# Performance work log

Measured on AMD Instinct MI355X. Metric: run time of the kernel, lower is better.

The kernel has to match this reference:

```python
import jax, jax.numpy as jnp
import numpy as np

H = 8
LN_EPS = 1e-5


def _layer_norm(t):
    # LayerNorm over last dim, no affine (elementwise_affine=False, bias=False)
    mu = jnp.mean(t, axis=-1, keepdims=True)
    var = jnp.var(t, axis=-1, keepdims=True)
    return (t - mu) / jnp.sqrt(var + LN_EPS)


def setup_inputs() -> dict:
    key = jax.random.key(0)
    ks = jax.random.split(key, 7)
    B, N, D, K = 2, 8192, 512, 32
    x = jax.random.normal(ks[0], (B, N, D), dtype=jnp.float32)
    idx = jax.random.randint(ks[1], (N, K), 0, N)
    s = 1.0 / np.sqrt(D)  # kaiming-ish init scale for stability
    Wq = jax.random.normal(ks[2], (D, D), dtype=jnp.float32) * s
    Wk = jax.random.normal(ks[3], (D, D), dtype=jnp.float32) * s
    Wv = jax.random.normal(ks[4], (D, D), dtype=jnp.float32) * s
    Wout = jax.random.normal(ks[5], (D, D), dtype=jnp.float32) * s
    bout = jnp.zeros((D,), dtype=jnp.float32)
    return {"x": x, "idx": idx, "Wq": Wq, "Wk": Wk, "Wv": Wv, "Wout": Wout, "bout": bout}


def reference(x, idx, Wq, Wk, Wv, Wout, bout):
    B, N, D = x.shape
    d_k = D // H

    def proj(W):
        # torch Linear: x @ W.T ; reshape to (B, H, N, d_k)
        return (x @ W.T).reshape(B, N, H, d_k).transpose(0, 2, 1, 3)

    Q, K, V = proj(Wq), proj(Wk), proj(Wv)
    # per-head LayerNorm on d_k (all heads identical since no affine params)
    Q = _layer_norm(Q)
    K = _layer_norm(K)

    # grouped (neighborhood) attention: gather K,V at neighbor indices
    Kg = K[:, :, idx]  # (B, H, N, k, d_k)
    Vg = V[:, :, idx]  # (B, H, N, k, d_k)
    scores = jnp.einsum('bhnd,bhnkd->bhnk', Q, Kg) / jnp.sqrt(jnp.asarray(d_k, x.dtype))
    attn = jax.nn.softmax(scores, axis=-1)
    out = jnp.einsum('bhnk,bhnkd->bhnd', attn, Vg)  # (B, H, N, d_k)

    out = out.transpose(0, 2, 1, 3).reshape(B, N, D)
    return out @ Wout.T + bout
```

## Files before the change

kernel.cpp:

```cpp
#include <hip/hip_runtime.h>
#include <hip/hip_bf16.h>
#include <math.h>

#define BB 2
#define NN 8192
#define DD 512
#define HH 8
#define DK 64
#define KNB 32
#define BN (BB*NN)
#define BHN (BB*HH*NN)

typedef __attribute__((ext_vector_type(8))) _Float16 f16x8;
typedef __attribute__((ext_vector_type(2))) _Float16 f16x2;
typedef __attribute__((ext_vector_type(4))) float f32x4;

#if __has_builtin(__builtin_amdgcn_fdot2)
#define HAS_FDOT2 1
#endif

__device__ __forceinline__ unsigned short f2h(float f) {
    return __builtin_bit_cast(unsigned short, (_Float16)f);
}
__device__ __forceinline__ f16x2 u2h2(unsigned u) {
    return __builtin_bit_cast(f16x2, u);
}
__device__ __forceinline__ float h2f_lo(unsigned u) {
    return (float)__builtin_bit_cast(_Float16, (unsigned short)(u & 0xffffu));
}
__device__ __forceinline__ float h2f_hi(unsigned u) {
    return (float)__builtin_bit_cast(_Float16, (unsigned short)(u >> 16));
}
__device__ __forceinline__ float dot2h(unsigned a, unsigned b, float c) {
#ifdef HAS_FDOT2
    return __builtin_amdgcn_fdot2(u2h2(a), u2h2(b), c, false);
#else
    c = fmaf(h2f_lo(a), h2f_lo(b), c);
    return fmaf(h2f_hi(a), h2f_hi(b), c);
#endif
}

__device__ __forceinline__ void gload_lds16(const void* gptr, void* lptr) {
    __builtin_amdgcn_global_load_lds(
        (const __attribute__((address_space(1))) unsigned int*)gptr,
        (__attribute__((address_space(3))) unsigned int*)lptr,
        16, 0, 0);
}

__global__ __launch_bounds__(256) void cvt_all(
    const float* __restrict__ x,
    const float* __restrict__ Wq, const float* __restrict__ Wk,
    const float* __restrict__ Wv, const float* __restrict__ Wo,
    unsigned short* __restrict__ Xb, unsigned short* __restrict__ Wfb,
    unsigned short* __restrict__ Wob)
{
    const int blk = blockIdx.x;
    const float* src;
    unsigned short* dst;
    int off;
    if (blk < 8192) {
        off = (blk * 256 + threadIdx.x) * 4;
        src = x; dst = Xb;
    } else {
        const int e = ((blk - 8192) * 256 + threadIdx.x) * 4;
        const int t = e >> 18;
        off = e & 262143;
        src = (t == 0) ? Wq : (t == 1) ? Wk : (t == 2) ? Wv : Wo;
        dst = (t < 3) ? (Wfb + (size_t)t * 262144) : Wob;
    }
    const float4 v = *(const float4*)(src + off);
    ushort4 u;
    u.x = f2h(v.x); u.y = f2h(v.y); u.z = f2h(v.z); u.w = f2h(v.w);
    *(ushort4*)(dst + off) = u;
}

__global__ __launch_bounds__(256) void gemm_qkv(
    const unsigned short* __restrict__ Xb, const unsigned short* __restrict__ Wfb,
    unsigned short* __restrict__ Qh, unsigned short* __restrict__ Kh,
    unsigned short* __restrict__ Vh)
{
    __shared__ unsigned short Als[128 * 32];
    __shared__ unsigned short Bls[128 * 32];
    const int tid  = threadIdx.x;
    const int wave = tid >> 6, lane = tid & 63;
    const int wm = wave >> 1, wn = wave & 1;
    const int quad = lane >> 4, r = lane & 15;
    const int row0 = blockIdx.x * 128;
    const int c0   = blockIdx.y * 128;

    f32x4 acc[4][4];
    #pragma unroll
    for (int i = 0; i < 4; ++i)
        #pragma unroll
        for (int j = 0; j < 4; ++j) acc[i][j] = (f32x4)0.f;

    const char* Ab = (const char*)Xb;
    const char* Bb = (const char*)Wfb;

    for (int k0 = 0; k0 < 512; k0 += 32) {
        __syncthreads();
        #pragma unroll
        for (int q = 0; q < 2; ++q) {
            const int li = q * 4096 + wave * 1024 + lane * 16;
            const int rr = li >> 6, off = li & 63;
            gload_lds16(Ab + (size_t)(row0 + rr) * 1024 + k0 * 2 + off,
                        (char*)Als + (q * 4096 + wave * 1024));
            gload_lds16(Bb + (size_t)(c0 + rr) * 1024 + k0 * 2 + off,
                        (char*)Bls + (q * 4096 + wave * 1024));
        }
        __syncthreads();

        f16x8 af[4], bf[4];
        #pragma unroll
        for (int i = 0; i < 4; ++i)
            af[i] = *(const f16x8*)(&Als[(wm * 64 + i * 16 + r) * 32 + quad * 8]);
        #pragma unroll
        for (int j = 0; j < 4; ++j)
            bf[j] = *(const f16x8*)(&Bls[(wn * 64 + j * 16 + r) * 32 + quad * 8]);
        #pragma unroll
        for (int i = 0; i < 4; ++i)
            #pragma unroll
            for (int j = 0; j < 4; ++j)
                acc[i][j] = __builtin_amdgcn_mfma_f32_16x16x32_f16(af[i], bf[j], acc[i][j], 0, 0, 0);
    }

    const int tensor = c0 >> 9;
    unsigned short* OutH = (tensor == 0) ? Qh : (tensor == 1) ? Kh : Vh;

    float mu[4][4], rs[4][4];
    if (tensor < 2) {
        #pragma unroll
        for (int i = 0; i < 4; ++i) {
            #pragma unroll
            for (int reg = 0; reg < 4; ++reg) {
                float sm = acc[i][0][reg] + acc[i][1][reg] + acc[i][2][reg] + acc[i][3][reg];
                sm += __shfl_xor(sm, 1); sm += __shfl_xor(sm, 2);
                sm += __shfl_xor(sm, 4); sm += __shfl_xor(sm, 8);
                const float muv = sm * (1.f / 64.f);
                float qv = 0.f;
                #pragma unroll
                for (int j = 0; j < 4; ++j) {
                    const float dv = acc[i][j][reg] - muv;
                    qv = fmaf(dv, dv, qv);
                }
                qv += __shfl_xor(qv, 1); qv += __shfl_xor(qv, 2);
                qv += __shfl_xor(qv, 4); qv += __shfl_xor(qv, 8);
                mu[i][reg] = muv;
                rs[i][reg] = rsqrtf(qv * (1.f / 64.f) + 1e-5f);
            }
        }
    }

    #pragma unroll
    for (int i = 0; i < 4; ++i) {
        #pragma unroll
        for (int j = 0; j < 4; ++j) {
            const int cc = (c0 & 511) + wn * 64 + j * 16 + r;
            const int h = cc >> 6, d = cc & 63;
            #pragma unroll
            for (int reg = 0; reg < 4; ++reg) {
                const int row = row0 + wm * 64 + i * 16 + quad * 4 + reg;
                const int b = row >> 13, n = row & 8191;
                float v = acc[i][j][reg];
                if (tensor < 2) v = (v - mu[i][reg]) * rs[i][reg];
                OutH[(((size_t)(b * HH + h) * NN + n) << 6) + d] = f2h(v);
            }
        }
    }
}

__global__ __launch_bounds__(256, 2) void attn(
    const unsigned short* __restrict__ Qh, const unsigned short* __restrict__ Kh,
    const unsigned short* __restrict__ Vh,
    const int* __restrict__ idx, unsigned short* __restrict__ Ob)
{
    __shared__ unsigned short Vls[4][2048];
    const int p = blockIdx.x;
    const int L = ((p & 7) << 12) | (p >> 3);
    const int wave = threadIdx.x >> 6;
    const int wid  = L * 4 + wave;
    const int lane = threadIdx.x & 63;
    const int bh = wid >> 13;
    const int n  = wid & 8191;
    const size_t base = (size_t)bh * NN * DK;

    const int g_all = idx[n * KNB + (lane & 31)];

    char* lw = (char*)Vls[wave];
    const char* Vbytes = (const char*)Vh + (base << 1);
    const int col16 = (lane & 7) * 16;
    const int pa = (lane >> 3) * 4;
    #pragma unroll
    for (int j = 0; j < 4; ++j) {
        const int gv = __builtin_amdgcn_ds_bpermute(pa + j * 32, g_all);
        gload_lds16(Vbytes + (size_t)(gv * 128) + col16, lw + j * 1024);
    }

    const int k    = lane >> 1;
    const int half = lane & 1;
    const int g    = __builtin_amdgcn_ds_bpermute(k * 4, g_all);

    const uint4* q4 = (const uint4*)(Qh + base + ((size_t)n << 6) + half * 32);
    const uint4* k4 = (const uint4*)(Kh + base + ((size_t)g << 6) + half * 32);
    float acc = 0.f;
    #pragma unroll
    for (int c = 0; c < 4; ++c) {
        const uint4 qa = q4[c], ka = k4[c];
        acc = dot2h(qa.x, ka.x, acc);
        acc = dot2h(qa.y, ka.y, acc);
        acc = dot2h(qa.z, ka.z, acc);
        acc = dot2h(qa.w, ka.w, acc);
    }
    float s = (acc + __shfl_xor(acc, 1)) * 0.125f;

    float m = s;
    #pragma unroll
    for (int off = 2; off <= 32; off <<= 1) m = fmaxf(m, __shfl_xor(m, off));
    const float e = __expf(s - m);
    float tot = e;
    #pragma unroll
    for (int off = 2; off <= 32; off <<= 1) tot += __shfl_xor(tot, off);
    const float pr = e / tot;

    const unsigned prh = (unsigned)f2h(pr);
    const unsigned pp = prh | (((unsigned)__shfl_xor((int)prh, 2)) << 16);

    asm volatile("s_waitcnt vmcnt(0)" ::: "memory");

    const int c2 = lane & 31, h2 = lane >> 5;
    const char* lb = lw + h2 * 2048 + c2 * 4;
    float o0 = 0.f, o1 = 0.f;
    #pragma unroll
    for (int j = 0; j < 8; ++j) {
        const unsigned vx = *(const unsigned*)(lb + j * 256);
        const unsigned vy = *(const unsigned*)(lb + j * 256 + 128);
        const unsigned ppj = (unsigned)__builtin_amdgcn_ds_bpermute(h2 * 128 + j * 16, (int)pp);
        const unsigned t0 = __builtin_amdgcn_perm(vx, vy, 0x01000504u);
        const unsigned t1 = __builtin_amdgcn_perm(vx, vy, 0x03020706u);
        o0 = dot2h(t0, ppj, o0);
        o1 = dot2h(t1, ppj, o1);
    }
    o0 += __shfl_xor(o0, 32);
    o1 += __shfl_xor(o1, 32);
    if (lane < 32) {
        const int b = bh >> 3, hh = bh & 7;
        const unsigned ov = (unsigned)f2h(o0) | ((unsigned)f2h(o1) << 16);
        *(unsigned*)(Ob + ((size_t)(b * NN + n)) * DD + hh * DK + 2 * c2) = ov;
    }
}

__global__ __launch_bounds__(256) void gemm_out(
    const unsigned short* __restrict__ Ob, const unsigned short* __restrict__ Wob,
    const float* __restrict__ bout, float* __restrict__ out)
{
    __shared__ unsigned short Als[128 * 32];
    __shared__ unsigned short Bls[128 * 32];
    const int tid  = threadIdx.x;
    const int wave = tid >> 6, lane = tid & 63;
    const int wm = wave >> 1, wn = wave & 1;
    const int quad = lane >> 4, r = lane & 15;
    const int row0 = blockIdx.x * 128;
    const int c0   = blockIdx.y * 128;

    f32x4 acc[4][4];
    #pragma unroll
    for (int i = 0; i < 4; ++i)
        #pragma unroll
        for (int j = 0; j < 4; ++j) acc[i][j] = (f32x4)0.f;

    const char* Ab = (const char*)Ob;
    const char* Bb = (const char*)Wob;

    for (int k0 = 0; k0 < 512; k0 += 32) {
        __syncthreads();
        #pragma unroll
        for (int q = 0; q < 2; ++q) {
            const int li = q * 4096 + wave * 1024 + lane * 16;
            const int rr = li >> 6, off = li & 63;
            gload_lds16(Ab + (size_t)(row0 + rr) * 1024 + k0 * 2 + off,
                        (char*)Als + (q * 4096 + wave * 1024));
            gload_lds16(Bb + (size_t)(c0 + rr) * 1024 + k0 * 2 + off,
                        (char*)Bls + (q * 4096 + wave * 1024));
        }
        __syncthreads();

        f16x8 af[4], bf[4];
        #pragma unroll
        for (int i = 0; i < 4; ++i)
            af[i] = *(const f16x8*)(&Als[(wm * 64 + i * 16 + r) * 32 + quad * 8]);
        #pragma unroll
        for (int j = 0; j < 4; ++j)
            bf[j] = *(const f16x8*)(&Bls[(wn * 64 + j * 16 + r) * 32 + quad * 8]);
        #pragma unroll
        for (int i = 0; i < 4; ++i)
            #pragma unroll
            for (int j = 0; j < 4; ++j)
                acc[i][j] = __builtin_amdgcn_mfma_f32_16x16x32_f16(af[i], bf[j], acc[i][j], 0, 0, 0);
    }

    #pragma unroll
    for (int i = 0; i < 4; ++i) {
        #pragma unroll
        for (int j = 0; j < 4; ++j) {
            const int colg = c0 + wn * 64 + j * 16 + r;
            const float bb = bout[colg];
            #pragma unroll
            for (int reg = 0; reg < 4; ++reg) {
                const int row = row0 + wm * 64 + i * 16 + quad * 4 + reg;
                out[((size_t)row << 9) + colg] = acc[i][j][reg] + bb;
            }
        }
    }
}

extern "C" void kernel_launch(void* const* d_in, const int* in_sizes, int n_in,
                              void* d_out, int out_size, void* d_ws, size_t ws_size,
                              hipStream_t stream)
{
    const float* x    = (const float*)d_in[0];
    const int*   idx  = (const int*)  d_in[1];
    const float* Wq   = (const float*)d_in[2];
    const float* Wk   = (const float*)d_in[3];
    const float* Wv   = (const float*)d_in[4];
    const float* Wout = (const float*)d_in[5];
    const float* bout = (const float*)d_in[6];

    char* ws = (char*)d_ws;
    unsigned short* Qh  = (unsigned short*)(ws);
    unsigned short* Kh  = (unsigned short*)(ws + 16777216);
    unsigned short* Vh  = (unsigned short*)(ws + 33554432);
    unsigned short* Xb  = (unsigned short*)(ws + 50331648);
    unsigned short* Ob  = Xb;
    unsigned short* Wfb = (unsigned short*)(ws + 67108864);
    unsigned short* Wob = (unsigned short*)(ws + 68681728);
    float* out = (float*)d_out;

    cvt_all<<<9216, 256, 0, stream>>>(x, Wq, Wk, Wv, Wout, Xb, Wfb, Wob);

    dim3 g1(BN / 128, 1536 / 128);
    gemm_qkv<<<g1, 256, 0, stream>>>(Xb, Wfb, Qh, Kh, Vh);

    attn<<<BHN / 4, 256, 0, stream>>>(Qh, Kh, Vh, idx, Ob);

    dim3 g2(BN / 128, 512 / 128);
    gemm_out<<<g2, 256, 0, stream>>>(Ob, Wob, bout, out);
}
```

Baseline: 221.7 us.

## Process eight queries per wave with double-buffered V neighbor prefetch into LDS

Each wave in the attention kernel now handles eight consecutive query rows instead of one, and the launch grid shrinks by a factor of eight. A second LDS buffer per wave holds the next row's gathered V neighbors: they are loaded asynchronously while the current row's QK dot products, softmax and PV accumulation run, with a partial vmcnt wait. The goal is to hide gather latency and amortize per-block launch and setup cost. The cost is twice the LDS per block and a longer serial dependency chain per wave, which may reduce the latency hiding that comes from having many waves resident.

```diff
diff --git a/kernel.cpp b/kernel.cpp
--- a/kernel.cpp
+++ b/kernel.cpp
@@ -174,78 +174,97 @@
     const unsigned short* __restrict__ Vh,
     const int* __restrict__ idx, unsigned short* __restrict__ Ob)
 {
-    __shared__ unsigned short Vls[4][2048];
+    __shared__ unsigned short Vls[4][2][2048];
     const int p = blockIdx.x;
-    const int L = ((p & 7) << 12) | (p >> 3);
     const int wave = threadIdx.x >> 6;
-    const int wid  = L * 4 + wave;
     const int lane = threadIdx.x & 63;
-    const int bh = wid >> 13;
-    const int n  = wid & 8191;
+    const int wid0 = ((p & 7) << 14) + ((p >> 3) << 5) + (wave << 3);
+    const int bh = wid0 >> 13;
+    const int n0 = wid0 & 8191;
     const size_t base = (size_t)bh * NN * DK;
 
-    const int g_all = idx[n * KNB + (lane & 31)];
-
-    char* lw = (char*)Vls[wave];
+    char* s0 = (char*)Vls[wave][0];
+    char* s1 = (char*)Vls[wave][1];
     const char* Vbytes = (const char*)Vh + (base << 1);
     const int col16 = (lane & 7) * 16;
-    const int pa = (lane >> 3) * 4;
+    const int pa  = (lane >> 3) * 4;
+    const int k    = lane >> 1;
+    const int half = lane & 1;
+    const int c2 = lane & 31, h2 = lane >> 5;
+    const int b = bh >> 3, hh = bh & 7;
+
+    int g_all = idx[n0 * KNB + (lane & 31)];
     #pragma unroll
     for (int j = 0; j < 4; ++j) {
         const int gv = __builtin_amdgcn_ds_bpermute(pa + j * 32, g_all);
-        gload_lds16(Vbytes + (size_t)(gv * 128) + col16, lw + j * 1024);
-    }
-
-    const int k    = lane >> 1;
-    const int half = lane & 1;
-    const int g    = __builtin_amdgcn_ds_bpermute(k * 4, g_all);
-
-    const uint4* q4 = (const uint4*)(Qh + base + ((size_t)n << 6) + half * 32);
-    const uint4* k4 = (const uint4*)(Kh + base + ((size_t)g << 6) + half * 32);
-    float acc = 0.f;
-    #pragma unroll
-    for (int c = 0; c < 4; ++c) {
-        const uint4 qa = q4[c], ka = k4[c];
-        acc = dot2h(qa.x, ka.x, acc);
-        acc = dot2h(qa.y, ka.y, acc);
-        acc = dot2h(qa.z, ka.z, acc);
-        acc = dot2h(qa.w, ka.w, acc);
-    }
-    float s = (acc + __shfl_xor(acc, 1)) * 0.125f;
-
-    float m = s;
-    #pragma unroll
-    for (int off = 2; off <= 32; off <<= 1) m = fmaxf(m, __shfl_xor(m, off));
-    const float e = __expf(s - m);
-    float tot = e;
-    #pragma unroll
-    for (int off = 2; off <= 32; off <<= 1) tot += __shfl_xor(tot, off);
-    const float pr = e / tot;
-
-    const unsigned prh = (unsigned)f2h(pr);
-    const unsigned pp = prh | (((unsigned)__shfl_xor((int)prh, 2)) << 16);
-
-    asm volatile("s_waitcnt vmcnt(0)" ::: "memory");
-
-    const int c2 = lane & 31, h2 = lane >> 5;
-    const char* lb = lw + h2 * 2048 + c2 * 4;
-    float o0 = 0.f, o1 = 0.f;
-    #pragma unroll
-    for (int j = 0; j < 8; ++j) {
-        const unsigned vx = *(const unsigned*)(lb + j * 256);
-        const unsigned vy = *(const unsigned*)(lb + j * 256 + 128);
-        const unsigned ppj = (unsigned)__builtin_amdgcn_ds_bpermute(h2 * 128 + j * 16, (int)pp);
-        const unsigned t0 = __builtin_amdgcn_perm(vx, vy, 0x01000504u);
-        const unsigned t1 = __builtin_amdgcn_perm(vx, vy, 0x03020706u);
-        o0 = dot2h(t0, ppj, o0);
-        o1 = dot2h(t1, ppj, o1);
-    }
-    o0 += __shfl_xor(o0, 32);
-    o1 += __shfl_xor(o1, 32);
-    if (lane < 32) {
-        const int b = bh >> 3, hh = bh & 7;
-        const unsigned ov = (unsigned)f2h(o0) | ((unsigned)f2h(o1) << 16);
-        *(unsigned*)(Ob + ((size_t)(b * NN + n)) * DD + hh * DK + 2 * c2) = ov;
+        gload_lds16(Vbytes + (size_t)(gv * 128) + col16, s0 + j * 1024);
+    }
+
+    #pragma unroll
+    for (int t = 0; t < 8; ++t) {
+        const int n = n0 + t;
+        char* cur = (t & 1) ? s1 : s0;
+        char* nxt = (t & 1) ? s0 : s1;
+
+        int g_next = 0;
+        if (t < 7) g_next = idx[(n + 1) * KNB + (lane & 31)];
+
+        const int g = __builtin_amdgcn_ds_bpermute(k * 4, g_all);
+        const uint4* q4 = (const uint4*)(Qh + base + ((size_t)n << 6) + half * 32);
+        const uint4* k4 = (const uint4*)(Kh + base + ((size_t)g << 6) + half * 32);
+        float acc = 0.f;
+        #pragma unroll
+        for (int c = 0; c < 4; ++c) {
+            const uint4 qa = q4[c], ka = k4[c];
+            acc = dot2h(qa.x, ka.x, acc);
+            acc = dot2h(qa.y, ka.y, acc);
+            acc = dot2h(qa.z, ka.z, acc);
+            acc = dot2h(qa.w, ka.w, acc);
+        }
+        float s = (acc + __shfl_xor(acc, 1)) * 0.125f;
+
+        float m = s;
+        #pragma unroll
+        for (int off = 2; off <= 32; off <<= 1) m = fmaxf(m, __shfl_xor(m, off));
+        const float e = __expf(s - m);
+        float tot = e;
+        #pragma unroll
+        for (int off = 2; off <= 32; off <<= 1) tot += __shfl_xor(tot, off);
+        const float pr = e / tot;
+
+        const unsigned prh = (unsigned)f2h(pr);
+        const unsigned pp = prh | (((unsigned)__shfl_xor((int)prh, 2)) << 16);
+
+        if (t < 7) {
+            #pragma unroll
+            for (int j = 0; j < 4; ++j) {
+                const int gv = __builtin_amdgcn_ds_bpermute(pa + j * 32, g_next);
+                gload_lds16(Vbytes + (size_t)(gv * 128) + col16, nxt + j * 1024);
+            }
+            asm volatile("s_waitcnt vmcnt(4)" ::: "memory");
+        } else {
+            asm volatile("s_waitcnt vmcnt(0)" ::: "memory");
+        }
+
+        const char* lb = cur + h2 * 2048 + c2 * 4;
+        float o0 = 0.f, o1 = 0.f;
+        #pragma unroll
+        for (int j = 0; j < 8; ++j) {
+            const unsigned vx = *(const unsigned*)(lb + j * 256);
+            const unsigned vy = *(const unsigned*)(lb + j * 256 + 128);
+            const unsigned ppj = (unsigned)__builtin_amdgcn_ds_bpermute(h2 * 128 + j * 16, (int)pp);
+            const unsigned t0 = __builtin_amdgcn_perm(vx, vy, 0x01000504u);
+            const unsigned t1 = __builtin_amdgcn_perm(vx, vy, 0x03020706u);
+            o0 = dot2h(t0, ppj, o0);
+            o1 = dot2h(t1, ppj, o1);
+        }
+        o0 += __shfl_xor(o0, 32);
+        o1 += __shfl_xor(o1, 32);
+        if (lane < 32) {
+            const unsigned ov = (unsigned)f2h(o0) | ((unsigned)f2h(o1) << 16);
+            *(unsigned*)(Ob + ((size_t)(b * NN + n)) * DD + hh * DK + 2 * c2) = ov;
+        }
+        g_all = g_next;
     }
 }
 
@@ -340,7 +359,7 @@
     dim3 g1(BN / 128, 1536 / 128);
     gemm_qkv<<<g1, 256, 0, stream>>>(Xb, Wfb, Qh, Kh, Vh);
 
-    attn<<<BHN / 4, 256, 0, stream>>>(Qh, Kh, Vh, idx, Ob);
+    attn<<<BHN / 32, 256, 0, stream>>>(Qh, Kh, Vh, idx, Ob);
 
     dim3 g2(BN / 128, 512 / 128);
     gemm_out<<<g2, 256, 0, stream>>>(Ob, Wob, bout, out);
```

Result: no change. 225.7 us (+1.8%).

## Load gathered V rows directly from global and drop softmax max reduction

Applied to the files above, without the earlier changes.

The attention kernel no longer stages the gathered V rows into LDS with async global-to-LDS copies. Each lane now reads its V elements straight from global memory inside the PV loop, using lane-permuted neighbor indices. The softmax skips the max-subtraction reduction, which relies on the scores being bounded because Q and K are layer-normalized. The QK dot product is split into two accumulator chains to shorten the dependency chain. Removing LDS can raise occupancy and saves the shuffles, but the V load latency may now be exposed late in the kernel instead of overlapping the QK work.

```diff
diff --git a/kernel.cpp b/kernel.cpp
--- a/kernel.cpp
+++ b/kernel.cpp
@@ -174,7 +174,6 @@
     const unsigned short* __restrict__ Vh,
     const int* __restrict__ idx, unsigned short* __restrict__ Ob)
 {
-    __shared__ unsigned short Vls[4][2048];
     const int p = blockIdx.x;
     const int L = ((p & 7) << 12) | (p >> 3);
     const int wave = threadIdx.x >> 6;
@@ -186,37 +185,37 @@
 
     const int g_all = idx[n * KNB + (lane & 31)];
 
-    char* lw = (char*)Vls[wave];
-    const char* Vbytes = (const char*)Vh + (base << 1);
-    const int col16 = (lane & 7) * 16;
-    const int pa = (lane >> 3) * 4;
-    #pragma unroll
-    for (int j = 0; j < 4; ++j) {
-        const int gv = __builtin_amdgcn_ds_bpermute(pa + j * 32, g_all);
-        gload_lds16(Vbytes + (size_t)(gv * 128) + col16, lw + j * 1024);
-    }
-
     const int k    = lane >> 1;
     const int half = lane & 1;
     const int g    = __builtin_amdgcn_ds_bpermute(k * 4, g_all);
 
     const uint4* q4 = (const uint4*)(Qh + base + ((size_t)n << 6) + half * 32);
     const uint4* k4 = (const uint4*)(Kh + base + ((size_t)g << 6) + half * 32);
-    float acc = 0.f;
-    #pragma unroll
-    for (int c = 0; c < 4; ++c) {
-        const uint4 qa = q4[c], ka = k4[c];
-        acc = dot2h(qa.x, ka.x, acc);
-        acc = dot2h(qa.y, ka.y, acc);
-        acc = dot2h(qa.z, ka.z, acc);
-        acc = dot2h(qa.w, ka.w, acc);
-    }
-    float s = (acc + __shfl_xor(acc, 1)) * 0.125f;
-
-    float m = s;
-    #pragma unroll
-    for (int off = 2; off <= 32; off <<= 1) m = fmaxf(m, __shfl_xor(m, off));
-    const float e = __expf(s - m);
+    float a0 = 0.f, a1 = 0.f;
+    {
+        const uint4 qa = q4[0], ka = k4[0];
+        a0 = dot2h(qa.x, ka.x, a0); a0 = dot2h(qa.y, ka.y, a0);
+        a0 = dot2h(qa.z, ka.z, a0); a0 = dot2h(qa.w, ka.w, a0);
+    }
+    {
+        const uint4 qa = q4[1], ka = k4[1];
+        a1 = dot2h(qa.x, ka.x, a1); a1 = dot2h(qa.y, ka.y, a1);
+        a1 = dot2h(qa.z, ka.z, a1); a1 = dot2h(qa.w, ka.w, a1);
+    }
+    {
+        const uint4 qa = q4[2], ka = k4[2];
+        a0 = dot2h(qa.x, ka.x, a0); a0 = dot2h(qa.y, ka.y, a0);
+        a0 = dot2h(qa.z, ka.z, a0); a0 = dot2h(qa.w, ka.w, a0);
+    }
+    {
+        const uint4 qa = q4[3], ka = k4[3];
+        a1 = dot2h(qa.x, ka.x, a1); a1 = dot2h(qa.y, ka.y, a1);
+        a1 = dot2h(qa.z, ka.z, a1); a1 = dot2h(qa.w, ka.w, a1);
+    }
+    const float acc = a0 + a1;
+    const float s = (acc + __shfl_xor(acc, 1)) * 0.125f;
+
+    const float e = __expf(s);
     float tot = e;
     #pragma unroll
     for (int off = 2; off <= 32; off <<= 1) tot += __shfl_xor(tot, off);
@@ -225,15 +224,15 @@
     const unsigned prh = (unsigned)f2h(pr);
     const unsigned pp = prh | (((unsigned)__shfl_xor((int)prh, 2)) << 16);
 
-    asm volatile("s_waitcnt vmcnt(0)" ::: "memory");
-
+    const char* Vbytes = (const char*)Vh + (base << 1);
     const int c2 = lane & 31, h2 = lane >> 5;
-    const char* lb = lw + h2 * 2048 + c2 * 4;
     float o0 = 0.f, o1 = 0.f;
     #pragma unroll
     for (int j = 0; j < 8; ++j) {
-        const unsigned vx = *(const unsigned*)(lb + j * 256);
-        const unsigned vy = *(const unsigned*)(lb + j * 256 + 128);
+        const int r0 = __builtin_amdgcn_ds_bpermute((h2 * 16 + 2 * j) * 4, g_all);
+        const int r1 = __builtin_amdgcn_ds_bpermute((h2 * 16 + 2 * j + 1) * 4, g_all);
+        const unsigned vx = *(const unsigned*)(Vbytes + (size_t)(r0 * 128) + c2 * 4);
+        const unsigned vy = *(const unsigned*)(Vbytes + (size_t)(r1 * 128) + c2 * 4);
         const unsigned ppj = (unsigned)__builtin_amdgcn_ds_bpermute(h2 * 128 + j * 16, (int)pp);
         const unsigned t0 = __builtin_amdgcn_perm(vx, vy, 0x01000504u);
         const unsigned t1 = __builtin_amdgcn_perm(vx, vy, 0x03020706u);
```

Measured after the change: 219.8 us. About the same (-0.9%).
